# Kernel optimization log

Measured on AMD Instinct MI355X. Metric: run time of the kernel, lower is better.

The kernel has to match this reference:

```python
import jax, jax.numpy as jnp
import numpy as np

NB_POOLS = 256


def setup_inputs() -> dict:
    key = jax.random.key(0)
    x = jax.random.normal(key, (32, 32, 32, 512), dtype=jnp.float32)
    return {"x": x}


def reference(x) -> jnp.ndarray:
    B, R, C, F = x.shape
    nb_maps = R * C
    x3 = x.reshape(B, nb_maps, F)
    # self-correlation: (B, nb_maps, nb_maps), normalized by feature count
    corr = jnp.einsum('bmf,bnf->bmn', x3, x3) / F
    corr = corr.reshape(B, R, C, nb_maps)
    # percentile ranks into the descending-sorted correlation values
    ranks = jnp.round(jnp.linspace(1.0, nb_maps - 1, NB_POOLS)).astype(jnp.int32)
    # full descending sort along last axis (matches tf.nn.top_k k=nb_maps)
    x_sort = -jnp.sort(-corr, axis=-1)
    x_pool = x_sort[..., ranks]  # (B, R, C, NB_POOLS)
    return x_pool
```

## Files before the change

### kernel.cpp

```cpp
#include <hip/hip_runtime.h>


#define NMAPS 1024
#define FDIM 512
#define TM 16
#define NT 256

typedef __attribute__((ext_vector_type(8))) short short8_t;
typedef __attribute__((ext_vector_type(4))) float f32x4;
typedef __attribute__((ext_vector_type(16))) float f32x16;
typedef _Float16 h2 __attribute__((ext_vector_type(2)));

#define SELD 0x03020504u
#define SELA 0x07060100u

__device__ __forceinline__ h2 h2min(h2 a, h2 b) { return __builtin_elementwise_min(a, b); }
__device__ __forceinline__ h2 h2max(h2 a, h2 b) { return __builtin_elementwise_max(a, b); }

__device__ __forceinline__ unsigned h2u(h2 x) { union { h2 h; unsigned u; } t; t.h = x; return t.u; }
__device__ __forceinline__ h2 u2h(unsigned x) { union { h2 h; unsigned u; } t; t.u = x; return t.h; }

__device__ __forceinline__ h2 h2swap(h2 v) {
  unsigned u = h2u(v);
  return u2h((u >> 16) | (u << 16));
}

__device__ __forceinline__ h2 h2shfl_xor(h2 v, int m) {
  union { h2 h; int i; } u;
  u.h = v;
  u.i = __shfl_xor(u.i, m, 64);
  return u.h;
}

__device__ __forceinline__ void ce_pair(h2& a, h2& b, bool d) {
  h2 mn = h2min(a, b), mx = h2max(a, b);
  a = d ? mx : mn;
  b = d ? mn : mx;
}

__device__ __forceinline__ h2 ce1(h2 w, unsigned sel) {
  h2 s = h2swap(w);
  h2 mn = h2min(w, s), mx = h2max(w, s);
#if __has_builtin(__builtin_amdgcn_perm)
  return u2h(__builtin_amdgcn_perm(h2u(mx), h2u(mn), sel));
#else
  h2 rd; rd[0] = mx[0]; rd[1] = mn[1];
  h2 ra; ra[0] = mn[0]; ra[1] = mx[1];
  return (sel == SELD) ? rd : ra;
#endif
}

__device__ __forceinline__ void intra_merge16(h2 w[8], bool d, unsigned sel) {
  ce_pair(w[0], w[4], d); ce_pair(w[1], w[5], d); ce_pair(w[2], w[6], d); ce_pair(w[3], w[7], d);
  ce_pair(w[0], w[2], d); ce_pair(w[1], w[3], d); ce_pair(w[4], w[6], d); ce_pair(w[5], w[7], d);
  ce_pair(w[0], w[1], d); ce_pair(w[2], w[3], d); ce_pair(w[4], w[5], d); ce_pair(w[6], w[7], d);
#pragma unroll
  for (int u = 0; u < 8; ++u) w[u] = ce1(w[u], sel);
}

__device__ __forceinline__ void sort16(h2 w[8], bool d, unsigned sd, unsigned si) {
  w[0] = ce1(w[0], sd); w[1] = ce1(w[1], si); w[2] = ce1(w[2], sd); w[3] = ce1(w[3], si);
  w[4] = ce1(w[4], sd); w[5] = ce1(w[5], si); w[6] = ce1(w[6], sd); w[7] = ce1(w[7], si);
  ce_pair(w[0], w[1], d); ce_pair(w[2], w[3], !d); ce_pair(w[4], w[5], d); ce_pair(w[6], w[7], !d);
  w[0] = ce1(w[0], sd); w[1] = ce1(w[1], sd); w[2] = ce1(w[2], si); w[3] = ce1(w[3], si);
  w[4] = ce1(w[4], sd); w[5] = ce1(w[5], sd); w[6] = ce1(w[6], si); w[7] = ce1(w[7], si);
  ce_pair(w[0], w[2], d); ce_pair(w[1], w[3], d); ce_pair(w[4], w[6], !d); ce_pair(w[5], w[7], !d);
  ce_pair(w[0], w[1], d); ce_pair(w[2], w[3], d); ce_pair(w[4], w[5], !d); ce_pair(w[6], w[7], !d);
  w[0] = ce1(w[0], sd); w[1] = ce1(w[1], sd); w[2] = ce1(w[2], sd); w[3] = ce1(w[3], sd);
  w[4] = ce1(w[4], si); w[5] = ce1(w[5], si); w[6] = ce1(w[6], si); w[7] = ce1(w[7], si);
  intra_merge16(w, d, sd);
}

__device__ __forceinline__ void merge32(h2 w[16], bool d) {
  const unsigned sel = d ? SELD : SELA;
#pragma unroll
  for (int u = 0; u < 8; ++u) ce_pair(w[u], w[u + 8], d);
#pragma unroll
  for (int u = 0; u < 16; ++u)
    if ((u & 4) == 0) ce_pair(w[u], w[u | 4], d);
#pragma unroll
  for (int u = 0; u < 16; ++u)
    if ((u & 2) == 0) ce_pair(w[u], w[u | 2], d);
#pragma unroll
  for (int u = 0; u < 16; ++u)
    if ((u & 1) == 0) ce_pair(w[u], w[u | 1], d);
#pragma unroll
  for (int u = 0; u < 16; ++u) w[u] = ce1(w[u], sel);
}

__device__ __forceinline__ void merge64(h2 w[32], bool d) {
  const unsigned sel = d ? SELD : SELA;
#pragma unroll
  for (int u = 0; u < 16; ++u) ce_pair(w[u], w[u + 16], d);
#pragma unroll
  for (int u = 0; u < 32; ++u)
    if ((u & 8) == 0) ce_pair(w[u], w[u | 8], d);
#pragma unroll
  for (int u = 0; u < 32; ++u)
    if ((u & 4) == 0) ce_pair(w[u], w[u | 4], d);
#pragma unroll
  for (int u = 0; u < 32; ++u)
    if ((u & 2) == 0) ce_pair(w[u], w[u | 2], d);
#pragma unroll
  for (int u = 0; u < 32; ++u)
    if ((u & 1) == 0) ce_pair(w[u], w[u | 1], d);
#pragma unroll
  for (int u = 0; u < 32; ++u) w[u] = ce1(w[u], sel);
}

template<int N>
__device__ __forceinline__ void cross_ceN(h2* w, int m, bool keepmax) {
#pragma unroll
  for (int u = 0; u < N; ++u) {
    h2 p = h2shfl_xor(w[u], m);
    h2 mn = h2min(w[u], p), mx = h2max(w[u], p);
    w[u] = keepmax ? mx : mn;
  }
}
__device__ __forceinline__ void cross_ce(h2 w[8], int m, bool keepmax) {
  cross_ceN<8>(w, m, keepmax);
}

template<int K>
__device__ __forceinline__ void bitonic_stage(h2 w8[8], int lane) {
  const bool laneDesc = (K >= 16) ? ((lane & (K >> 4)) == 0) : true;
#pragma unroll
  for (int j = 512; j >= 16; j >>= 1) {
    if (j > (K >> 1)) continue;
    const int m = j >> 4;
    const bool keepmax = (((lane & m) == 0) == laneDesc);
#pragma unroll
    for (int u = 0; u < 8; ++u) {
      h2 p = h2shfl_xor(w8[u], m);
      h2 mn = h2min(w8[u], p), mx = h2max(w8[u], p);
      w8[u] = keepmax ? mx : mn;
    }
  }
#pragma unroll
  for (int j = 8; j >= 2; j >>= 1) {
    if (j > (K >> 1)) continue;
    const int jw = j >> 1;
#pragma unroll
    for (int u = 0; u < 8; ++u) {
      if ((u & jw) == 0) {
        const int v = u | jw;
        const bool desc = (K <= 8) ? (((2 * u) & K) == 0) : laneDesc;
        h2 mn = h2min(w8[u], w8[v]), mx = h2max(w8[u], w8[v]);
        w8[u] = desc ? mx : mn;
        w8[v] = desc ? mn : mx;
      }
    }
  }
#pragma unroll
  for (int u = 0; u < 8; ++u) {
    const bool desc = (K <= 8) ? (((2 * u) & K) == 0) : laneDesc;
    h2 s = h2swap(w8[u]);
    h2 mn = h2min(w8[u], s), mx = h2max(w8[u], s);
    h2 rd = (h2){mx[0], mn[1]};
    h2 ra = (h2){mn[0], mx[1]};
    w8[u] = desc ? rd : ra;
  }
}

template<int K>
__device__ __forceinline__ void bitonic_stage_tail4(h2 A[8], h2 B[8], h2 C[8], h2 Dw[8],
                                                    int lane) {
  const bool laneDesc = ((lane & (K >> 4)) == 0);
#pragma unroll
  for (int j = 512; j >= 16; j >>= 1) {
    if (j > (K >> 1)) continue;
    const int m = j >> 4;
    const bool km = (((lane & m) == 0) == laneDesc);
    cross_ce(A, m, km);
    cross_ce(B, m, km);
    cross_ce(C, m, km);
    cross_ce(Dw, m, km);
  }
  const unsigned sel = laneDesc ? SELD : SELA;
  intra_merge16(A, laneDesc, sel);
  intra_merge16(B, laneDesc, sel);
  intra_merge16(C, laneDesc, sel);
  intra_merge16(Dw, laneDesc, sel);
}

__device__ __forceinline__ void run_bitonic(h2 w8[8], int lane) {
  bitonic_stage<2>(w8, lane);
  bitonic_stage<4>(w8, lane);
  bitonic_stage<8>(w8, lane);
  bitonic_stage<16>(w8, lane);
  bitonic_stage<32>(w8, lane);
  bitonic_stage<64>(w8, lane);
  bitonic_stage<128>(w8, lane);
  bitonic_stage<256>(w8, lane);
  bitonic_stage<512>(w8, lane);
  bitonic_stage<1024>(w8, lane);
}

__global__ __launch_bounds__(256) void cvt_bf16_kernel(const float* __restrict__ x,
                                                       short* __restrict__ xw, int n8) {
  int i = blockIdx.x * 256 + threadIdx.x;
  if (i >= n8) return;
  const float4* x4 = reinterpret_cast<const float4*>(x);
  float4 a = x4[i * 2], c = x4[i * 2 + 1];
  float f[8] = {a.x, a.y, a.z, a.w, c.x, c.y, c.z, c.w};
  union { short8_t v; short s[8]; } o;
#pragma unroll
  for (int j = 0; j < 8; ++j) {
    unsigned u = __float_as_uint(f[j]);
    u += 0x7fffu + ((u >> 16) & 1u);
    o.s[j] = (short)(u >> 16);
  }
  reinterpret_cast<short8_t*>(xw)[i] = o.v;
}

__device__ __forceinline__ int swzr(int r) { return ((r >> 1) ^ (r >> 3)) & 3; }

__global__ __launch_bounds__(256) void corr_gemm_tiled(const short* __restrict__ xw,
                                                       unsigned* __restrict__ corrW) {
  __shared__ short Bsm[2][128 * 32];
  const int tid = threadIdx.x;
  int b, tile;
  if (gridDim.x == 2048) {
    const int bid = blockIdx.x;
    const int xcd = bid & 7;
    const int j = bid >> 3;
    b = (j >> 6) * 8 + xcd;
    tile = j & 63;
  } else {
    b = blockIdx.x >> 6;
    tile = blockIdx.x & 63;
  }
  const int it = tile >> 3, jt = tile & 7;
  const int i0 = it * 128, j0 = jt * 128;
  const int lane = tid & 63;
  const int w = tid >> 6;
  const int lr32 = lane & 31;
  const int hi = lane >> 5;
  const short* Xb = xw + (size_t)b * NMAPS * FDIM;

  int srcOff[2], dstOff[2];
  {
    const int idxs[2] = {tid, tid + 256};
#pragma unroll
    for (int rp = 0; rp < 2; ++rp) {
      const int r = idxs[rp] >> 2;
      const int s = (idxs[rp] & 3) ^ swzr(r);
      srcOff[rp] = r * FDIM + s * 8;
      dstOff[rp] = idxs[rp] * 8;
    }
  }

  int bOff[4][2];
#pragma unroll
  for (int tc = 0; tc < 4; ++tc) {
    const int rb = tc * 32 + lr32;
#pragma unroll
    for (int ks = 0; ks < 2; ++ks)
      bOff[tc][ks] = rb * 32 + (((2 * ks + hi) ^ swzr(rb)) * 8);
  }

  const short* gAbase = Xb + (size_t)(i0 + w * 32 + lr32) * FDIM + hi * 8;

  f32x16 acc[4];
#pragma unroll
  for (int tc = 0; tc < 4; ++tc)
#pragma unroll
    for (int q = 0; q < 16; ++q) acc[tc][q] = 0.f;

#define STAGE_B(buf, kt)                                                               \
  {                                                                                    \
    _Pragma("unroll") for (int rp = 0; rp < 2; ++rp) {                                 \
      const short* gB = Xb + (size_t)j0 * FDIM + srcOff[rp] + (kt) * 32;               \
      __builtin_amdgcn_global_load_lds(                                                \
          (const __attribute__((address_space(1))) unsigned*)gB,                       \
          (__attribute__((address_space(3))) unsigned*)(Bsm[buf] + dstOff[rp]), 16,    \
          0, 0);                                                                       \
    }                                                                                  \
  }
#define LOAD_A(d0, d1, kt)                                                             \
  {                                                                                    \
    d0 = *reinterpret_cast<const short8_t*>(gAbase + (kt) * 32);                       \
    d1 = *reinterpret_cast<const short8_t*>(gAbase + (kt) * 32 + 16);                  \
  }
#define SBAR() __builtin_amdgcn_sched_barrier(0)
#define BARRIER()                      \
  {                                    \
    SBAR();                            \
    __builtin_amdgcn_s_barrier();      \
    SBAR();                            \
  }

  short8_t aCur0, aCur1, aNxt0, aNxt1;
  STAGE_B(0, 0);
  LOAD_A(aCur0, aCur1, 0);

  for (int kt = 0; kt < 16; ++kt) {
    const int cur = kt & 1;
    BARRIER();
    if (kt < 15) {
      STAGE_B(cur ^ 1, kt + 1);
      LOAD_A(aNxt0, aNxt1, kt + 1);
      SBAR();
      asm volatile("s_waitcnt vmcnt(4)" ::: "memory");
    } else {
      SBAR();
      asm volatile("s_waitcnt vmcnt(0)" ::: "memory");
    }
    BARRIER();

#pragma unroll
    for (int ks = 0; ks < 2; ++ks) {
      const short8_t a = (ks == 0) ? aCur0 : aCur1;
      short8_t bf[4];
#pragma unroll
      for (int tc = 0; tc < 4; ++tc)
        bf[tc] = *reinterpret_cast<const short8_t*>(Bsm[cur] + bOff[tc][ks]);
#pragma unroll
      for (int tc = 0; tc < 4; ++tc)
        acc[tc] = __builtin_amdgcn_mfma_f32_32x32x16_bf16(bf[tc], a, acc[tc], 0, 0, 0);
    }
    aCur0 = aNxt0;
    aCur1 = aNxt1;
  }
#undef STAGE_B
#undef LOAD_A
#undef BARRIER
#undef SBAR

  {
    const bool D = ((jt & 1) == 0);
    h2 W[32];
#pragma unroll
    for (int tc = 0; tc < 4; ++tc)
#pragma unroll
      for (int q = 0; q < 8; ++q)
        W[tc * 8 + q] = (h2){(_Float16)acc[tc][2 * q], (_Float16)acc[tc][2 * q + 1]};
    sort16(W, true, SELD, SELA);
    sort16(W + 8, false, SELA, SELD);
    merge32(W, true);
    sort16(W + 16, true, SELD, SELA);
    sort16(W + 24, false, SELA, SELD);
    merge32(W + 16, false);
    merge64(W, hi == 0);
    cross_ceN<32>(W, 32, (hi == 0) == D);
    merge64(W, D);
    const size_t roww = ((size_t)b * NMAPS + i0 + w * 32 + lr32) * 512;
    const int wq = (j0 >> 1) + hi * 32;
#pragma unroll
    for (int g = 0; g < 8; ++g) {
      union { h2 h[4]; uint4 u; } s;
#pragma unroll
      for (int q = 0; q < 4; ++q) s.h[q] = W[g * 4 + q];
      *reinterpret_cast<uint4*>(corrW + roww + wq + g * 4) = s.u;
    }
  }
}

__global__ __launch_bounds__(256) void sort_rows_kernel(const unsigned* __restrict__ corrW,
                                                        float* __restrict__ out) {
  const int tid = threadIdx.x;
  const int lane = tid & 63;
  const int rA = blockIdx.x * 16 + (tid >> 6) * 4;
  const uint4* pa = reinterpret_cast<const uint4*>(corrW + (size_t)rA * 512);
  const uint4* pb = reinterpret_cast<const uint4*>(corrW + (size_t)(rA + 1) * 512);
  const uint4* pc = reinterpret_cast<const uint4*>(corrW + (size_t)(rA + 2) * 512);
  const uint4* pd = reinterpret_cast<const uint4*>(corrW + (size_t)(rA + 3) * 512);

  h2 A[8], B[8], C[8], Dw[8];
  {
    union { uint4 u; h2 h[4]; } t0, t1;
    t0.u = pa[lane * 2]; t1.u = pa[lane * 2 + 1];
    A[0] = t0.h[0]; A[1] = t0.h[1]; A[2] = t0.h[2]; A[3] = t0.h[3];
    A[4] = t1.h[0]; A[5] = t1.h[1]; A[6] = t1.h[2]; A[7] = t1.h[3];
    t0.u = pb[lane * 2]; t1.u = pb[lane * 2 + 1];
    B[0] = t0.h[0]; B[1] = t0.h[1]; B[2] = t0.h[2]; B[3] = t0.h[3];
    B[4] = t1.h[0]; B[5] = t1.h[1]; B[6] = t1.h[2]; B[7] = t1.h[3];
    t0.u = pc[lane * 2]; t1.u = pc[lane * 2 + 1];
    C[0] = t0.h[0]; C[1] = t0.h[1]; C[2] = t0.h[2]; C[3] = t0.h[3];
    C[4] = t1.h[0]; C[5] = t1.h[1]; C[6] = t1.h[2]; C[7] = t1.h[3];
    t0.u = pd[lane * 2]; t1.u = pd[lane * 2 + 1];
    Dw[0] = t0.h[0]; Dw[1] = t0.h[1]; Dw[2] = t0.h[2]; Dw[3] = t0.h[3];
    Dw[4] = t1.h[0]; Dw[5] = t1.h[1]; Dw[6] = t1.h[2]; Dw[7] = t1.h[3];
  }

  bitonic_stage_tail4<256>(A, B, C, Dw, lane);
  bitonic_stage_tail4<512>(A, B, C, Dw, lane);
  bitonic_stage_tail4<1024>(A, B, C, Dw, lane);

  float* oa = out + (size_t)rA * 256;
  float* ob = oa + 256;
  float* oc = ob + 256;
  float* od = oc + 256;
#pragma unroll
  for (int u = 0; u < 8; ++u) {
#pragma unroll
    for (int hh = 0; hh < 2; ++hh) {
      const int i = lane * 16 + 2 * u + hh;
      const int p = (int)rint((double)(i - 1) * (255.0 / 1022.0));
      const int rk = (int)rint(1.0 + (double)p * (1022.0 / 255.0));
      if (rk == i) {
        oa[p] = (float)A[u][hh] * (1.f / FDIM);
        ob[p] = (float)B[u][hh] * (1.f / FDIM);
        oc[p] = (float)C[u][hh] * (1.f / FDIM);
        od[p] = (float)Dw[u][hh] * (1.f / FDIM);
      }
    }
  }
}

__global__ __launch_bounds__(NT) void selfcorr_mfma_kernel(const short* __restrict__ xw,
                                                           float* __restrict__ out) {
  __shared__ alignas(16) h2 SH[TM * 512];
  const int tid = threadIdx.x;
  const int b = blockIdx.y;
  const int m0 = blockIdx.x * TM;
  const int lane = tid & 63;
  const int wid = tid >> 6;
  const int lr = lane & 15;
  const int kg = lane >> 4;
  const int wc = wid * 256;
  const short* Xb = xw + (size_t)b * NMAPS * FDIM;

  f32x4 acc[16];
#pragma unroll
  for (int t = 0; t < 16; ++t) acc[t] = (f32x4){0.f, 0.f, 0.f, 0.f};

  for (int kk = 0; kk < 16; ++kk) {
    const short8_t* base = reinterpret_cast<const short8_t*>(Xb + kk * 32 + kg * 8);
    short8_t afrag = base[(size_t)(m0 + lr) * 64];
    short8_t bfrag[16];
#pragma unroll
    for (int t = 0; t < 16; ++t) bfrag[t] = base[(size_t)(wc + t * 16 + lr) * 64];
#pragma unroll
    for (int t = 0; t < 16; ++t)
      acc[t] = __builtin_amdgcn_mfma_f32_16x16x32_bf16(bfrag[t], afrag, acc[t], 0, 0, 0);
  }

  {
    const int xorv = (lr & 7) << 2;
#pragma unroll
    for (int t = 0; t < 16; ++t) {
      h2 lo = (h2){(_Float16)(acc[t][0] * (1.f / FDIM)), (_Float16)(acc[t][1] * (1.f / FDIM))};
      h2 hi = (h2){(_Float16)(acc[t][2] * (1.f / FDIM)), (_Float16)(acc[t][3] * (1.f / FDIM))};
      const int W = (wc >> 1) + t * 8 + kg * 2;
      const int phys = lr * 512 + (W ^ xorv);
      union { h2 h[2]; uint2 u; } pk;
      pk.h[0] = lo; pk.h[1] = hi;
      *reinterpret_cast<uint2*>(&SH[phys]) = pk.u;
    }
  }
  __syncthreads();

  const int rowbase = wid * 4;
  for (int rr = rowbase; rr < rowbase + 4; ++rr) {
    const int rx = (rr & 7) << 2;
    h2 w8[8];
#pragma unroll
    for (int q = 0; q < 2; ++q) {
      const int p4 = rr * 512 + ((lane * 8 + q * 4) ^ rx);
      union { uint4 u; h2 h[4]; } un;
      un.u = *reinterpret_cast<const uint4*>(&SH[p4]);
      w8[q * 4 + 0] = un.h[0]; w8[q * 4 + 1] = un.h[1];
      w8[q * 4 + 2] = un.h[2]; w8[q * 4 + 3] = un.h[3];
    }
    run_bitonic(w8, lane);
#pragma unroll
    for (int q = 0; q < 2; ++q) {
      const int p4 = rr * 512 + ((lane * 8 + q * 4) ^ rx);
      union { uint4 u; h2 h[4]; } un;
      un.h[0] = w8[q * 4 + 0]; un.h[1] = w8[q * 4 + 1];
      un.h[2] = w8[q * 4 + 2]; un.h[3] = w8[q * 4 + 3];
      *reinterpret_cast<uint4*>(&SH[p4]) = un.u;
    }
  }
  __builtin_amdgcn_wave_barrier();

#pragma unroll
  for (int i = 0; i < 16; ++i) {
    const int rr = rowbase + (i >> 2);
    const int p = lane + ((i & 3) << 6);
    const int rank = (int)rint(1.0 + (double)p * (1022.0 / 255.0));
    const int Wr = (rank >> 1) ^ ((rr & 7) << 2);
    h2 hv = SH[rr * 512 + Wr];
    out[((size_t)(b * NMAPS + m0 + rr) << 8) + p] = (float)hv[rank & 1];
  }
}

__device__ __forceinline__ int sw4(int row, int c4) {
  return (row << 8) | (c4 ^ ((c4 >> 3) & 7));
}
__device__ __forceinline__ void ce(float& a, float& b, bool desc) {
  float mn = fminf(a, b);
  float mx = fmaxf(a, b);
  a = desc ? mx : mn;
  b = desc ? mn : mx;
}

__global__ __launch_bounds__(NT) void selfcorr_pool_kernel(const float* __restrict__ x,
                                                           float* __restrict__ out) {
  __shared__ float lds[TM * NMAPS];
  float4* S4 = reinterpret_cast<float4*>(lds);
  const int tid = threadIdx.x;
  const int b = blockIdx.y;
  const int m0 = blockIdx.x * TM;
  const float4* Xb = reinterpret_cast<const float4*>(x) + (size_t)b * NMAPS * (FDIM / 4);

  float4* A4 = reinterpret_cast<float4*>(lds);
#pragma unroll
  for (int idx = tid; idx < TM * (FDIM / 4); idx += NT) {
    A4[idx] = Xb[(m0 + (idx >> 7)) * 128 + (idx & 127)];
  }
  __syncthreads();

  float acc[TM][4];
#pragma unroll
  for (int m = 0; m < TM; ++m)
#pragma unroll
    for (int j = 0; j < 4; ++j) acc[m][j] = 0.0f;

  float4 nb0 = Xb[(tid + 0) * 128];
  float4 nb1 = Xb[(tid + 256) * 128];
  float4 nb2 = Xb[(tid + 512) * 128];
  float4 nb3 = Xb[(tid + 768) * 128];
  for (int k4 = 0; k4 < 128; ++k4) {
    float4 b0 = nb0, b1 = nb1, b2 = nb2, b3 = nb3;
    const int kn = (k4 < 127) ? (k4 + 1) : 127;
    nb0 = Xb[(tid + 0) * 128 + kn];
    nb1 = Xb[(tid + 256) * 128 + kn];
    nb2 = Xb[(tid + 512) * 128 + kn];
    nb3 = Xb[(tid + 768) * 128 + kn];
#pragma unroll
    for (int m = 0; m < TM; ++m) {
      float4 a = A4[m * 128 + k4];
      acc[m][0] += a.x * b0.x + a.y * b0.y + a.z * b0.z + a.w * b0.w;
      acc[m][1] += a.x * b1.x + a.y * b1.y + a.z * b1.z + a.w * b1.w;
      acc[m][2] += a.x * b2.x + a.y * b2.y + a.z * b2.z + a.w * b2.w;
      acc[m][3] += a.x * b3.x + a.y * b3.y + a.z * b3.z + a.w * b3.w;
    }
  }
  __syncthreads();

#pragma unroll
  for (int m = 0; m < TM; ++m) {
#pragma unroll
    for (int j = 0; j < 4; ++j) {
      const int n = tid + (j << 8);
      lds[sw4(m, n >> 2) * 4 + (n & 3)] = acc[m][j] * (1.0f / FDIM);
    }
  }
  __syncthreads();

#pragma unroll
  for (int c = 0; c < 2; ++c) {
    const int cid = tid + (c << 8);
    const int row = cid >> 5;
    const int chunk = cid & 31;
    float r[32];
#pragma unroll
    for (int q = 0; q < 8; ++q) {
      float4 t = S4[sw4(row, (chunk << 3) + q)];
      r[q * 4 + 0] = t.x; r[q * 4 + 1] = t.y; r[q * 4 + 2] = t.z; r[q * 4 + 3] = t.w;
    }
    const bool D = ((chunk & 1) == 0);
#pragma unroll
    for (int k2 = 2; k2 <= 32; k2 <<= 1) {
#pragma unroll
      for (int j = k2 >> 1; j > 0; j >>= 1) {
#pragma unroll
        for (int i = 0; i < 32; ++i) {
          if ((i & j) == 0) ce(r[i], r[i | j], ((i & k2) == 0) ? D : !D);
        }
      }
    }
#pragma unroll
    for (int q = 0; q < 8; ++q) {
      S4[sw4(row, (chunk << 3) + q)] =
          make_float4(r[q * 4 + 0], r[q * 4 + 1], r[q * 4 + 2], r[q * 4 + 3]);
    }
  }
  __syncthreads();

  for (int k = 64; k <= NMAPS; k <<= 1) {
    for (int j = k >> 1; j >= 32; j >>= 1) {
      const int j4 = j >> 2;
      const int kq = k >> 2;
#pragma unroll
      for (int q = 0; q < 8; ++q) {
        const int g = tid + (q << 8);
        const int row = g >> 7;
        const int v = g & 127;
        const int i4 = ((v & ~(j4 - 1)) << 1) | (v & (j4 - 1));
        const bool desc = ((i4 & kq) == 0);
        const int ia = sw4(row, i4);
        const int ib = sw4(row, i4 + j4);
        float4 va = S4[ia];
        float4 vb = S4[ib];
        float4 lo, hi;
        lo.x = fminf(va.x, vb.x); hi.x = fmaxf(va.x, vb.x);
        lo.y = fminf(va.y, vb.y); hi.y = fmaxf(va.y, vb.y);
        lo.z = fminf(va.z, vb.z); hi.z = fmaxf(va.z, vb.z);
        lo.w = fminf(va.w, vb.w); hi.w = fmaxf(va.w, vb.w);
        S4[ia] = desc ? hi : lo;
        S4[ib] = desc ? lo : hi;
      }
      __syncthreads();
    }
#pragma unroll
    for (int c = 0; c < 2; ++c) {
      const int cid = tid + (c << 8);
      const int row = cid >> 5;
      const int chunk = cid & 31;
      const bool D = (((chunk << 5) & k) == 0);
      float r[32];
#pragma unroll
      for (int q = 0; q < 8; ++q) {
        float4 t = S4[sw4(row, (chunk << 3) + q)];
        r[q * 4 + 0] = t.x; r[q * 4 + 1] = t.y; r[q * 4 + 2] = t.z; r[q * 4 + 3] = t.w;
      }
#pragma unroll
      for (int j = 16; j > 0; j >>= 1) {
#pragma unroll
        for (int i = 0; i < 32; ++i) {
          if ((i & j) == 0) ce(r[i], r[i | j], D);
        }
      }
#pragma unroll
      for (int q = 0; q < 8; ++q) {
        S4[sw4(row, (chunk << 3) + q)] =
            make_float4(r[q * 4 + 0], r[q * 4 + 1], r[q * 4 + 2], r[q * 4 + 3]);
      }
    }
    __syncthreads();
  }

  const int p = tid;
  const int rank = (int)rint(1.0 + (double)p * (1022.0 / 255.0));
#pragma unroll
  for (int m = 0; m < TM; ++m) {
    out[((size_t)(b * NMAPS + m0 + m) << 8) + p] = lds[sw4(m, rank >> 2) * 4 + (rank & 3)];
  }
}

extern "C" void kernel_launch(void* const* d_in, const int* in_sizes, int n_in,
                              void* d_out, int out_size, void* d_ws, size_t ws_size,
                              hipStream_t stream) {
  const float* x = reinterpret_cast<const float*>(d_in[0]);
  float* out = reinterpret_cast<float*>(d_out);
  const int nelem = in_sizes[0];
  const int B = nelem / (NMAPS * FDIM);
  const size_t need_split = (size_t)nelem * 2 + (size_t)B * NMAPS * NMAPS * 2;
  if (ws_size >= need_split) {
    short* xw = reinterpret_cast<short*>(d_ws);
    unsigned* corrW = reinterpret_cast<unsigned*>((char*)d_ws + (size_t)nelem * 2);
    const int n8 = nelem / 8;
    hipLaunchKernelGGL(cvt_bf16_kernel, dim3((n8 + 255) / 256), dim3(256), 0, stream, x, xw, n8);
    hipLaunchKernelGGL(corr_gemm_tiled, dim3(64 * B), dim3(256), 0, stream, xw, corrW);
    hipLaunchKernelGGL(sort_rows_kernel, dim3(B * NMAPS / 16), dim3(256), 0, stream, corrW, out);
  } else if (ws_size >= (size_t)nelem * 2) {
    short* xw = reinterpret_cast<short*>(d_ws);
    const int n8 = nelem / 8;
    hipLaunchKernelGGL(cvt_bf16_kernel, dim3((n8 + 255) / 256), dim3(256), 0, stream, x, xw, n8);
    hipLaunchKernelGGL(selfcorr_mfma_kernel, dim3(NMAPS / TM, B), dim3(NT), 0, stream, xw, out);
  } else {
    hipLaunchKernelGGL(selfcorr_pool_kernel, dim3(NMAPS / TM, B), dim3(NT), 0, stream, x, out);
  }
}
```

Before: 150.9 us.

## Fuse fp32-to-bf16 conversion into correlation GEMM tile loads

```diff
diff --git a/kernel.cpp b/kernel.cpp
--- a/kernel.cpp
+++ b/kernel.cpp
@@ -30,6 +30,21 @@
   u.h = v;
   u.i = __shfl_xor(u.i, m, 64);
   return u.h;
+}
+
+__device__ __forceinline__ unsigned cvt2bf(float lo, float hi) {
+  unsigned r;
+  asm volatile("v_cvt_pk_bf16_f32 %0, %1, %2" : "=v"(r) : "v"(lo), "v"(hi));
+  return r;
+}
+
+__device__ __forceinline__ short8_t cvt8bf(f32x4 a, f32x4 b) {
+  union { unsigned u[4]; short8_t s; } o;
+  o.u[0] = cvt2bf(a[0], a[1]);
+  o.u[1] = cvt2bf(a[2], a[3]);
+  o.u[2] = cvt2bf(b[0], b[1]);
+  o.u[3] = cvt2bf(b[2], b[3]);
+  return o.s;
 }
 
 __device__ __forceinline__ void ce_pair(h2& a, h2& b, bool d) {
@@ -215,7 +230,7 @@
 
 __device__ __forceinline__ int swzr(int r) { return ((r >> 1) ^ (r >> 3)) & 3; }
 
-__global__ __launch_bounds__(256) void corr_gemm_tiled(const short* __restrict__ xw,
+__global__ __launch_bounds__(256) void corr_gemm_fused(const float* __restrict__ xf,
                                                        unsigned* __restrict__ corrW) {
   __shared__ short Bsm[2][128 * 32];
   const int tid = threadIdx.x;
@@ -236,7 +251,7 @@
   const int w = tid >> 6;
   const int lr32 = lane & 31;
   const int hi = lane >> 5;
-  const short* Xb = xw + (size_t)b * NMAPS * FDIM;
+  const float* Xb = xf + (size_t)b * NMAPS * FDIM;
 
   int srcOff[2], dstOff[2];
   {
@@ -259,7 +274,7 @@
       bOff[tc][ks] = rb * 32 + (((2 * ks + hi) ^ swzr(rb)) * 8);
   }
 
-  const short* gAbase = Xb + (size_t)(i0 + w * 32 + lr32) * FDIM + hi * 8;
+  const float* gAbase = Xb + (size_t)(i0 + w * 32 + lr32) * FDIM + hi * 8;
 
   f32x16 acc[4];
 #pragma unroll
@@ -267,65 +282,61 @@
 #pragma unroll
     for (int q = 0; q < 16; ++q) acc[tc][q] = 0.f;
 
-#define STAGE_B(buf, kt)                                                               \
+  f32x4 bF[4], aF[4];
+
+#define LOADF(kt)                                                                      \
   {                                                                                    \
     _Pragma("unroll") for (int rp = 0; rp < 2; ++rp) {                                 \
-      const short* gB = Xb + (size_t)j0 * FDIM + srcOff[rp] + (kt) * 32;               \
-      __builtin_amdgcn_global_load_lds(                                                \
-          (const __attribute__((address_space(1))) unsigned*)gB,                       \
-          (__attribute__((address_space(3))) unsigned*)(Bsm[buf] + dstOff[rp]), 16,    \
-          0, 0);                                                                       \
+      const float* gB = Xb + (size_t)j0 * FDIM + srcOff[rp] + (kt) * 32;               \
+      bF[2 * rp] = *reinterpret_cast<const f32x4*>(gB);                                \
+      bF[2 * rp + 1] = *reinterpret_cast<const f32x4*>(gB + 4);                        \
     }                                                                                  \
-  }
-#define LOAD_A(d0, d1, kt)                                                             \
+    aF[0] = *reinterpret_cast<const f32x4*>(gAbase + (kt) * 32);                       \
+    aF[1] = *reinterpret_cast<const f32x4*>(gAbase + (kt) * 32 + 4);                   \
+    aF[2] = *reinterpret_cast<const f32x4*>(gAbase + (kt) * 32 + 16);                  \
+    aF[3] = *reinterpret_cast<const f32x4*>(gAbase + (kt) * 32 + 20);                  \
+  }
+#define CVTWRITE(buf, a0, a1)                                                          \
   {                                                                                    \
-    d0 = *reinterpret_cast<const short8_t*>(gAbase + (kt) * 32);                       \
-    d1 = *reinterpret_cast<const short8_t*>(gAbase + (kt) * 32 + 16);                  \
-  }
-#define SBAR() __builtin_amdgcn_sched_barrier(0)
-#define BARRIER()                      \
-  {                                    \
-    SBAR();                            \
-    __builtin_amdgcn_s_barrier();      \
-    SBAR();                            \
+    _Pragma("unroll") for (int rp = 0; rp < 2; ++rp) {                                 \
+      short8_t bs = cvt8bf(bF[2 * rp], bF[2 * rp + 1]);                                \
+      *reinterpret_cast<short8_t*>(Bsm[buf] + dstOff[rp]) = bs;                        \
+    }                                                                                  \
+    a0 = cvt8bf(aF[0], aF[1]);                                                         \
+    a1 = cvt8bf(aF[2], aF[3]);                                                         \
   }
 
   short8_t aCur0, aCur1, aNxt0, aNxt1;
-  STAGE_B(0, 0);
-  LOAD_A(aCur0, aCur1, 0);
+  LOADF(0);
+  CVTWRITE(0, aCur0, aCur1);
+  LOADF(1);
+  __syncthreads();
 
   for (int kt = 0; kt < 16; ++kt) {
     const int cur = kt & 1;
-    BARRIER();
     if (kt < 15) {
-      STAGE_B(cur ^ 1, kt + 1);
-      LOAD_A(aNxt0, aNxt1, kt + 1);
-      SBAR();
-      asm volatile("s_waitcnt vmcnt(4)" ::: "memory");
-    } else {
-      SBAR();
-      asm volatile("s_waitcnt vmcnt(0)" ::: "memory");
-    }
-    BARRIER();
+      CVTWRITE(cur ^ 1, aNxt0, aNxt1);
+      __syncthreads();
+      if (kt < 14) LOADF(kt + 2);
+    }
 
 #pragma unroll
     for (int ks = 0; ks < 2; ++ks) {
       const short8_t a = (ks == 0) ? aCur0 : aCur1;
-      short8_t bf[4];
+      short8_t bf2[4];
 #pragma unroll
       for (int tc = 0; tc < 4; ++tc)
-        bf[tc] = *reinterpret_cast<const short8_t*>(Bsm[cur] + bOff[tc][ks]);
+        bf2[tc] = *reinterpret_cast<const short8_t*>(Bsm[cur] + bOff[tc][ks]);
 #pragma unroll
       for (int tc = 0; tc < 4; ++tc)
-        acc[tc] = __builtin_amdgcn_mfma_f32_32x32x16_bf16(bf[tc], a, acc[tc], 0, 0, 0);
+        acc[tc] = __builtin_amdgcn_mfma_f32_32x32x16_bf16(bf2[tc], a, acc[tc], 0, 0, 0);
     }
     aCur0 = aNxt0;
     aCur1 = aNxt1;
-  }
-#undef STAGE_B
-#undef LOAD_A
-#undef BARRIER
-#undef SBAR
+    if (kt < 15) __syncthreads();
+  }
+#undef LOADF
+#undef CVTWRITE
 
   {
     const bool D = ((jt & 1) == 0);
@@ -648,13 +659,10 @@
   float* out = reinterpret_cast<float*>(d_out);
   const int nelem = in_sizes[0];
   const int B = nelem / (NMAPS * FDIM);
-  const size_t need_split = (size_t)nelem * 2 + (size_t)B * NMAPS * NMAPS * 2;
-  if (ws_size >= need_split) {
-    short* xw = reinterpret_cast<short*>(d_ws);
-    unsigned* corrW = reinterpret_cast<unsigned*>((char*)d_ws + (size_t)nelem * 2);
-    const int n8 = nelem / 8;
-    hipLaunchKernelGGL(cvt_bf16_kernel, dim3((n8 + 255) / 256), dim3(256), 0, stream, x, xw, n8);
-    hipLaunchKernelGGL(corr_gemm_tiled, dim3(64 * B), dim3(256), 0, stream, xw, corrW);
+  const size_t need_fused = (size_t)B * NMAPS * NMAPS * 2;
+  if (ws_size >= need_fused) {
+    unsigned* corrW = reinterpret_cast<unsigned*>(d_ws);
+    hipLaunchKernelGGL(corr_gemm_fused, dim3(64 * B), dim3(256), 0, stream, x, corrW);
     hipLaunchKernelGGL(sort_rows_kernel, dim3(B * NMAPS / 16), dim3(256), 0, stream, corrW, out);
   } else if (ws_size >= (size_t)nelem * 2) {
     short* xw = reinterpret_cast<short*>(d_ws);
```

Result: slower. 169.3 us (+12.2%).
